# Optimization experiments

Measured on AMD Instinct MI355X. Metric: run time of the kernel, lower is better.

Reference implementation:

```python
import jax, jax.numpy as jnp
import numpy as np

F = 3          # features
E = 2 * F      # transformer d_model
H = F          # n_heads (head_dim = 2)
FF = 2048      # torch TransformerEncoderLayer default dim_feedforward
OUT = 4
STRIDE = 2
N_BATCH = 16
T_LEN = 2046
LN_EPS = 1e-5


def setup_inputs() -> dict:
    key = jax.random.key(0)
    ks = iter(jax.random.split(key, 48))

    def p(shape, s=0.1):
        return jax.random.normal(next(ks), shape, dtype=jnp.float32) * s

    inp = {
        "x": jax.random.normal(next(ks), (N_BATCH, T_LEN, F), dtype=jnp.float32),
        # multi-scale depthwise conv kernels/biases
        "k64": p((8, F, 64)), "b64": p((8, F)),
        "k16": p((F, 16)), "b16": p((F,)),
        "k8": p((F, 8)), "b8": p((F,)),
        # stage-2 width-3 channel convs
        "kw3": p((F, 3)), "bw3": p((F,)),
        "km3": p((F, 3)), "bm3": p((F,)),
        "kn3": p((F, 3)), "bn3": p((F,)),
        # hidden FCs
        "fc1_w": p((6 * F, 12 * F)), "fc1_b": p((6 * F,)),
        "fc2_w": p((E, 6 * F)), "fc2_b": p((E,)),
        # 2 transformer encoder layers (stacked along leading dim)
        "inw": p((2, 3 * E, E)), "inb": p((2, 3 * E)),
        "ow": p((2, E, E)), "ob": p((2, E)),
        "l1w": jnp.ones((2, E), jnp.float32), "l1b": jnp.zeros((2, E), jnp.float32),
        "l2w": jnp.ones((2, E), jnp.float32), "l2b": jnp.zeros((2, E), jnp.float32),
        "f1w": p((2, FF, E)), "f1b": p((2, FF)),
        "f2w": p((2, E, FF)), "f2b": p((2, E)),
        # output head
        "out1_w": p((7, E)), "out1_b": p((7,)),
        "out2_w": p((OUT, 7)),
    }
    return inp


def _ln(y, w, b):
    mu = y.mean(-1, keepdims=True)
    var = ((y - mu) ** 2).mean(-1, keepdims=True)
    return (y - mu) / jnp.sqrt(var + LN_EPS) * w + b


def _conv3_same(y, k, b):
    # depthwise width-3 'same' conv over seq dim; y:(N,L,F), k:(F,3), b:(F,)
    yp = jnp.pad(y, ((0, 0), (1, 1), (0, 0)))
    return k[:, 0] * yp[:, :-2] + k[:, 1] * yp[:, 1:-1] + k[:, 2] * yp[:, 2:] + b


def _forward(x, k64, b64, k16, b16, k8, b8, kw3, bw3, km3, bm3, kn3, bn3,
             fc1_w, fc1_b, fc2_w, fc2_b, inw, inb, ow, ob,
             l1w, l1b, l2w, l2b, f1w, f1b, f2w, f2b, out1_w, out1_b, out2_w):
    N, T, _ = x.shape
    PAD = 40
    px = jnp.pad(x, ((0, 0), (PAD, PAD), (0, 0)))
    W = T // STRIDE + 1
    centers = PAD + 1 + STRIDE * jnp.arange(W)  # wide window centers
    starts = centers - 32
    relu = jax.nn.relu

    # wide: 8 depthwise width-64 kernels per center -> (N, 8W, F)
    wwin = px[:, centers[:, None] + jnp.arange(-32, 32), :]        # (N,W,64,F)
    wide = jnp.einsum('nwtf,kft->nwkf', wwin, k64) + b64[None, None]
    wide = wide.reshape(N, 8 * W, F)  # center-major, kernel-minor (loop order)

    # mid: width-16 kernel at 8 centers per window -> (N, 8W, F)
    mid_c = (starts[:, None] + 8 * jnp.arange(8)).reshape(-1)
    mwin = px[:, mid_c[:, None] + jnp.arange(-8, 8), :]            # (N,8W,16,F)
    mid = jnp.einsum('nctf,ft->ncf', mwin, k16) + b16

    # narrow: width-8 kernel at 32 centers per window, then maxpool4 -> (N, 8W, F)
    nar_c = (starts[:, None] + 2 * jnp.arange(32)).reshape(-1)
    nwin = px[:, nar_c[:, None] + jnp.arange(-4, 4), :]            # (N,32W,8,F)
    nar = jnp.einsum('nctf,ft->ncf', nwin, k8) + b8
    nar = nar.reshape(N, 8 * W, 4, F).max(axis=2)

    wide = 5.0 * relu(wide)  # residual=0, dropout=0 -> drop is identity
    mid = relu(mid)
    nar = relu(nar)

    wide = relu(_conv3_same(wide, kw3, bw3))
    mid = relu(_conv3_same(mid, km3, bm3))
    nar = relu(_conv3_same(nar, kn3, bn3))

    def pool2(y):  # MaxPool1d(2) over seq dim
        return y.reshape(N, 4 * W, 2, F).max(axis=2)
    wide, mid, nar = pool2(wide), pool2(mid), pool2(nar)

    S = W  # (4W) // 4 blocks

    def blocks(y):  # (N,4W,F) -> (N,S,4F), time-major flatten per block
        return y.reshape(N, S, 4 * F)
    flat = jnp.concatenate([blocks(wide), blocks(mid), blocks(nar)], axis=-1)

    h = relu(flat @ fc1_w.T + fc1_b)  # residual=0 -> (1-residual)*h + 0
    h = relu(h @ fc2_w.T + fc2_b)     # (N,S,E)
    seq = jnp.transpose(h, (1, 0, 2))  # (S,N,E), torch seq-first layout

    d = E // H
    scale = 1.0 / jnp.sqrt(jnp.float32(d))
    for l in range(2):  # post-LN TransformerEncoder, 2 layers
        qkv = seq @ inw[l].T + inb[l]                 # (S,N,3E)
        q, k_, v = jnp.split(qkv, 3, axis=-1)
        q = q.reshape(S, N, H, d)
        k_ = k_.reshape(S, N, H, d)
        v = v.reshape(S, N, H, d)
        att = jnp.einsum('snhd,tnhd->nhst', q, k_) * scale
        p_att = jax.nn.softmax(att, axis=-1)
        o = jnp.einsum('nhst,tnhd->snhd', p_att, v).reshape(S, N, E)
        o = o @ ow[l].T + ob[l]
        seq = _ln(seq + o, l1w[l], l1b[l])
        ff = relu(seq @ f1w[l].T + f1b[l]) @ f2w[l].T + f2b[l]
        seq = _ln(seq + ff, l2w[l], l2b[l])

    pooled = relu(seq.mean(axis=0))           # AvgPool1d over full seq -> (N,E)
    o1 = relu(pooled @ out1_w.T + out1_b)
    logits = o1 @ out2_w.T                    # no bias
    return jax.nn.log_softmax(logits, axis=1)


def reference(x, k64, b64, k16, b16, k8, b8, kw3, bw3, km3, bm3, kn3, bn3,
              fc1_w, fc1_b, fc2_w, fc2_b, inw, inb, ow, ob,
              l1w, l1b, l2w, l2b, f1w, f1b, f2w, f2b, out1_w, out1_b, out2_w):
    return _forward(x, k64, b64, k16, b16, k8, b8, kw3, bw3, km3, bm3, kn3, bn3,
                    fc1_w, fc1_b, fc2_w, fc2_b, inw, inb, ow, ob,
                    l1w, l1b, l2w, l2b, f1w, f1b, f2w, f2b, out1_w, out1_b, out2_w)
```

## Files before the change

kernel.cpp:

```cpp
#include <hip/hip_runtime.h>
#include <math.h>


#define NB 16
#define TL 2046
#define SL 1024
#define ED 6

__device__ __forceinline__ float relu_(float a){ return fmaxf(a, 0.f); }
__device__ __forceinline__ float fexp2_(float x){ return __builtin_amdgcn_exp2f(x); }

__global__ __launch_bounds__(192) void frontend_kernel(
  const float* __restrict__ x, const float* __restrict__ k64,
  const float* __restrict__ b64, const float* __restrict__ k16, const float* __restrict__ b16,
  const float* __restrict__ k8,  const float* __restrict__ b8,
  const float* __restrict__ kw3, const float* __restrict__ bw3,
  const float* __restrict__ km3, const float* __restrict__ bm3,
  const float* __restrict__ kn3, const float* __restrict__ bn3,
  const float* __restrict__ fc1w, const float* __restrict__ fc1b,
  const float* __restrict__ fc2w, const float* __restrict__ fc2b,
  const float* __restrict__ f1w, const float* __restrict__ f1b,
  const float* __restrict__ f2w,
  float* __restrict__ fcc, float* __restrict__ seq)
{
  __shared__ float xt[3][200];
  __shared__ float k64s[3*64*8];
  __shared__ float flat_s[64][44];
  __shared__ float h1_s[64][20];
  const int tid  = threadIdx.x;
  const int f    = tid >> 6;
  const int lane = tid & 63;
  const int n    = blockIdx.x >> 4;
  const int s0   = (blockIdx.x & 15) << 6;
  const int s    = s0 + lane;

  for (int i = blockIdx.x*192 + tid; i < 2*2048*16; i += 256*192){
    int l = i >> 15, r = i & 32767, j = r >> 4, c = r & 15;
    float v = 0.f;
    if (c < 6)       v = f1w[(l*2048 + j)*6 + c];
    else if (c == 6) v = f1b[l*2048 + j];
    else if (c >= 8 && c < 14) v = f2w[(l*6 + (c-8))*2048 + j];
    fcc[i] = v;
  }

  for (int i = tid; i < 600; i += 192){
    int ff = i / 200, pos = i - ff*200;
    int xp = 2*s0 - 39 + pos;
    xt[ff][pos] = (xp >= 0 && xp < TL) ? x[(n*TL + xp)*3 + ff] : 0.f;
  }
  for (int i = tid; i < 1536; i += 192){
    int ff = i >> 9, r = i & 511, t = r >> 3, k = r & 7;
    k64s[i] = k64[k*192 + ff*64 + t];
  }
  __syncthreads();

  float xr[74];
  {
    const int b = 2*lane;
    #pragma unroll
    for (int i = 0; i < 74; i++) xr[i] = xt[f][b + i];
  }

  float accw[8], acc_e0, acc_e1;
  #pragma unroll
  for (int k = 0; k < 8; k++) accw[k] = b64[k*3 + f];
  acc_e0 = accw[7]; acc_e1 = accw[0];
  {
    const float* kp = &k64s[f*512];
    #pragma unroll
    for (int t = 0; t < 64; t++){
      float4 wa = *(const float4*)(kp + t*8);
      float4 wb = *(const float4*)(kp + t*8 + 4);
      float xm = xr[8 + t];
      accw[0] = fmaf(xm, wa.x, accw[0]);
      accw[1] = fmaf(xm, wa.y, accw[1]);
      accw[2] = fmaf(xm, wa.z, accw[2]);
      accw[3] = fmaf(xm, wa.w, accw[3]);
      accw[4] = fmaf(xm, wb.x, accw[4]);
      accw[5] = fmaf(xm, wb.y, accw[5]);
      accw[6] = fmaf(xm, wb.z, accw[6]);
      accw[7] = fmaf(xm, wb.w, accw[7]);
      acc_e0 = fmaf(xr[6 + t],  wb.w, acc_e0);
      acc_e1 = fmaf(xr[10 + t], wa.x, acc_e1);
    }
  }
  float yw[10];
  yw[0] = (s > 0) ? 5.f*relu_(acc_e0) : 0.f;
  #pragma unroll
  for (int c = 1; c <= 8; c++) yw[c] = 5.f*relu_(accw[c-1]);
  yw[9] = (s < 1023) ? 5.f*relu_(acc_e1) : 0.f;

  float w16r[16];
  #pragma unroll
  for (int t = 0; t < 16; t++) w16r[t] = k16[f*16 + t];
  const float bb16 = b16[f];
  float ym[10];
  #pragma unroll
  for (int ci = 0; ci < 10; ci++){
    const int b = (ci == 0) ? 54 : ((ci == 9) ? 2 : 8*(ci-1));
    float a = bb16;
    #pragma unroll
    for (int t = 0; t < 16; t++) a = fmaf(xr[b + t], w16r[t], a);
    ym[ci] = relu_(a);
  }
  if (s == 0)    ym[0] = 0.f;
  if (s == 1023) ym[9] = 0.f;

  float w8r[8];
  #pragma unroll
  for (int t = 0; t < 8; t++) w8r[t] = k8[f*8 + t];
  const float bb8 = b8[f];
  float yn[10];
  #pragma unroll
  for (int ci = 0; ci < 10; ci++){
    float m = -3.0e38f;
    #pragma unroll
    for (int j2 = 0; j2 < 4; j2++){
      const int b = (ci == 0) ? (58 + 2*j2)
                  : ((ci == 9) ? (6 + 2*j2)
                               : (4 + 2*(4*(ci-1) + j2)));
      float a = bb8;
      #pragma unroll
      for (int t = 0; t < 8; t++) a = fmaf(xr[b + t], w8r[t], a);
      m = fmaxf(m, a);
    }
    yn[ci] = relu_(m);
  }
  if (s == 0)    yn[0] = 0.f;
  if (s == 1023) yn[9] = 0.f;

  {
    float c0 = kw3[f*3], c1 = kw3[f*3+1], c2 = kw3[f*3+2], bb = bw3[f];
    #pragma unroll
    for (int q = 0; q < 4; q++){
      float z0 = relu_(fmaf(c0, yw[2*q],   fmaf(c1, yw[2*q+1], fmaf(c2, yw[2*q+2], bb))));
      float z1 = relu_(fmaf(c0, yw[2*q+1], fmaf(c1, yw[2*q+2], fmaf(c2, yw[2*q+3], bb))));
      flat_s[lane][q*3 + f] = fmaxf(z0, z1);
    }
  }
  {
    float c0 = km3[f*3], c1 = km3[f*3+1], c2 = km3[f*3+2], bb = bm3[f];
    #pragma unroll
    for (int q = 0; q < 4; q++){
      float z0 = relu_(fmaf(c0, ym[2*q],   fmaf(c1, ym[2*q+1], fmaf(c2, ym[2*q+2], bb))));
      float z1 = relu_(fmaf(c0, ym[2*q+1], fmaf(c1, ym[2*q+2], fmaf(c2, ym[2*q+3], bb))));
      flat_s[lane][12 + q*3 + f] = fmaxf(z0, z1);
    }
  }
  {
    float c0 = kn3[f*3], c1 = kn3[f*3+1], c2 = kn3[f*3+2], bb = bn3[f];
    #pragma unroll
    for (int q = 0; q < 4; q++){
      float z0 = relu_(fmaf(c0, yn[2*q],   fmaf(c1, yn[2*q+1], fmaf(c2, yn[2*q+2], bb))));
      float z1 = relu_(fmaf(c0, yn[2*q+1], fmaf(c1, yn[2*q+2], fmaf(c2, yn[2*q+3], bb))));
      flat_s[lane][24 + q*3 + f] = fmaxf(z0, z1);
    }
  }
  __syncthreads();

  #pragma unroll
  for (int oi = 0; oi < 6; oi++){
    const int o = 6*f + oi;
    float acc = fc1b[o];
    const float4* wrow = (const float4*)(fc1w + o*36);
    const float4* frow = (const float4*)(&flat_s[lane][0]);
    #pragma unroll
    for (int i = 0; i < 9; i++){
      float4 wv = wrow[i], fv = frow[i];
      acc = fmaf(wv.x, fv.x, acc); acc = fmaf(wv.y, fv.y, acc);
      acc = fmaf(wv.z, fv.z, acc); acc = fmaf(wv.w, fv.w, acc);
    }
    h1_s[lane][o] = relu_(acc);
  }
  __syncthreads();

  #pragma unroll
  for (int ei = 0; ei < 2; ei++){
    const int e = 2*f + ei;
    float acc = fc2b[e];
    #pragma unroll
    for (int o = 0; o < 18; o++) acc = fmaf(h1_s[lane][o], fc2w[e*18 + o], acc);
    seq[(n*SL + s)*ED + e] = relu_(acc);
  }
}

__global__ __launch_bounds__(256) void attn_kernel(
  const float* __restrict__ seq, const float* __restrict__ inw,
  const float* __restrict__ inb, float* __restrict__ att_out, int layer)
{
  __shared__ float4 kv[1024];
  const int tid = threadIdx.x;
  const int bid = blockIdx.x;
  const int n = bid / 48;
  const int r = bid % 48;
  const int h = r >> 4;
  const int stile = r & 15;
  const float* W = inw + layer*108;
  const float* B = inb + layer*18;
  const int h2 = 2*h;
  const float* seqn = seq + n*SL*ED;
  const float SC = 1.0201265650432017f;

  float wk0[6], wk1[6], wv0[6], wv1[6];
  #pragma unroll
  for (int e = 0; e < 6; e++){
    wk0[e] = W[(6 + h2)*6 + e];  wk1[e] = W[(7 + h2)*6 + e];
    wv0[e] = W[(12 + h2)*6 + e]; wv1[e] = W[(13 + h2)*6 + e];
  }
  const float bk0 = B[6 + h2], bk1 = B[7 + h2], bv0 = B[12 + h2], bv1 = B[13 + h2];

  for (int i = tid; i < 1024; i += 256){
    const int t = (i & 3)*256 + (i >> 2);
    const float* sr = seqn + t*6;
    float a0 = sr[0], a1 = sr[1], a2 = sr[2], a3 = sr[3], a4 = sr[4], a5 = sr[5];
    float k0 = bk0 + a0*wk0[0] + a1*wk0[1] + a2*wk0[2] + a3*wk0[3] + a4*wk0[4] + a5*wk0[5];
    float k1 = bk1 + a0*wk1[0] + a1*wk1[1] + a2*wk1[2] + a3*wk1[3] + a4*wk1[4] + a5*wk1[5];
    float v0 = bv0 + a0*wv0[0] + a1*wv0[1] + a2*wv0[2] + a3*wv0[3] + a4*wv0[4] + a5*wv0[5];
    float v1 = bv1 + a0*wv1[0] + a1*wv1[1] + a2*wv1[2] + a3*wv1[3] + a4*wv1[4] + a5*wv1[5];
    kv[i] = make_float4(k0*SC, k1*SC, v0, v1);
  }

  const int srow = stile*64 + (tid >> 2);
  const int q = tid & 3;
  float q0, q1;
  {
    const float* sr = seqn + srow*6;
    float a0 = sr[0], a1 = sr[1], a2 = sr[2], a3 = sr[3], a4 = sr[4], a5 = sr[5];
    q0 = B[h2]   + a0*W[h2*6]     + a1*W[h2*6+1]     + a2*W[h2*6+2]     + a3*W[h2*6+3]     + a4*W[h2*6+4]     + a5*W[h2*6+5];
    q1 = B[h2+1] + a0*W[(h2+1)*6] + a1*W[(h2+1)*6+1] + a2*W[(h2+1)*6+2] + a3*W[(h2+1)*6+3] + a4*W[(h2+1)*6+4] + a5*W[(h2+1)*6+5];
  }
  __syncthreads();

  float l = 0.f, o0 = 0.f, o1 = 0.f;
  #pragma unroll 8
  for (int it = 0; it < 256; it++){
    float4 K = kv[it*4 + q];
    float sc = fmaf(q0, K.x, q1*K.y);
    float p  = fexp2_(sc);
    l += p;
    o0 = fmaf(p, K.z, o0);
    o1 = fmaf(p, K.w, o1);
  }
  l  += __shfl_xor(l, 1);  l  += __shfl_xor(l, 2);
  o0 += __shfl_xor(o0, 1); o0 += __shfl_xor(o0, 2);
  o1 += __shfl_xor(o1, 1); o1 += __shfl_xor(o1, 2);
  if (q == 0){
    float inv = 1.0f / l;
    float* orow = att_out + (n*SL + srow)*ED + h2;
    orow[0] = o0*inv; orow[1] = o1*inv;
  }
}

__global__ __launch_bounds__(256) void ff_kernel(
  const float* __restrict__ seq_in, const float* __restrict__ att,
  const float* __restrict__ fcc,
  const float* __restrict__ ow, const float* __restrict__ ob,
  const float* __restrict__ l1w, const float* __restrict__ l1b,
  float* __restrict__ seq_mid, float* __restrict__ ffp, int layer)
{
  __shared__ float wc[512][16];
  __shared__ float sM[128][6];
  const int tid   = threadIdx.x;
  const int tile  = blockIdx.x >> 2;
  const int slice = blockIdx.x & 3;
  const int tok0  = tile * 128;

  const float4* FC = (const float4*)(fcc + (size_t)(layer*2048 + slice*512)*16);
  for (int i = tid; i < 2048; i += 256)
    ((float4*)wc)[i] = FC[i];

  if (tid < 128){
    const int token = tok0 + tid;
    const float* a  = att + token*6;
    const float* W  = ow + layer*36;
    float av[6];
    #pragma unroll
    for (int e = 0; e < 6; e++) av[e] = a[e];
    float y[6]; float mu = 0.f;
    #pragma unroll
    for (int e = 0; e < 6; e++){
      float o = ob[layer*6 + e];
      #pragma unroll
      for (int e2 = 0; e2 < 6; e2++) o = fmaf(av[e2], W[e*6 + e2], o);
      y[e] = seq_in[token*6 + e] + o;
      mu += y[e];
    }
    mu *= (1.f/6.f);
    float var = 0.f;
    #pragma unroll
    for (int e = 0; e < 6; e++){ float d = y[e] - mu; var = fmaf(d, d, var); }
    var *= (1.f/6.f);
    float rstd = rsqrtf(var + 1e-5f);
    #pragma unroll
    for (int e = 0; e < 6; e++)
      sM[tid][e] = (y[e] - mu)*rstd*l1w[layer*6 + e] + l1b[layer*6 + e];
  }
  __syncthreads();

  const int w = tid >> 6, lane = tid & 63, tp = lane >> 2, ss = lane & 3;

  float sv[8][6];
  {
    const float* sp = &sM[tp*8][0];
    #pragma unroll
    for (int t = 0; t < 8; t++)
      #pragma unroll
      for (int e = 0; e < 6; e++) sv[t][e] = sp[t*6 + e];
  }
  float acc[8][6];
  #pragma unroll
  for (int t = 0; t < 8; t++)
    #pragma unroll
    for (int e = 0; e < 6; e++) acc[t][e] = 0.f;

  const int rb = w*128 + ss;
  #pragma unroll 2
  for (int i = 0; i < 32; i++){
    const float4* wr = (const float4*)&wc[rb + i*4][0];
    float4 w0 = wr[0], w1 = wr[1], w2 = wr[2], w3 = wr[3];
    #pragma unroll
    for (int t = 0; t < 8; t++){
      float h = w1.z;
      h = fmaf(sv[t][0], w0.x, h); h = fmaf(sv[t][1], w0.y, h);
      h = fmaf(sv[t][2], w0.z, h); h = fmaf(sv[t][3], w0.w, h);
      h = fmaf(sv[t][4], w1.x, h); h = fmaf(sv[t][5], w1.y, h);
      h = relu_(h);
      acc[t][0] = fmaf(h, w2.x, acc[t][0]); acc[t][1] = fmaf(h, w2.y, acc[t][1]);
      acc[t][2] = fmaf(h, w2.z, acc[t][2]); acc[t][3] = fmaf(h, w2.w, acc[t][3]);
      acc[t][4] = fmaf(h, w3.x, acc[t][4]); acc[t][5] = fmaf(h, w3.y, acc[t][5]);
    }
  }

  #pragma unroll
  for (int t = 0; t < 8; t++)
    #pragma unroll
    for (int e = 0; e < 6; e++){
      acc[t][e] += __shfl_xor(acc[t][e], 1);
      acc[t][e] += __shfl_xor(acc[t][e], 2);
    }
  __syncthreads();
  float* red = (float*)wc;
  if (ss == 0){
    #pragma unroll
    for (int t = 0; t < 8; t++)
      #pragma unroll
      for (int e = 0; e < 6; e++) red[(w*16 + tp)*48 + t*6 + e] = acc[t][e];
  }
  __syncthreads();
  for (int i = tid; i < 768; i += 256){
    const int tl = i / 6, e = i - tl*6;
    const int rtp = tl >> 3, rt = tl & 7;
    float sum = red[(0*16 + rtp)*48 + rt*6 + e]
              + red[(1*16 + rtp)*48 + rt*6 + e]
              + red[(2*16 + rtp)*48 + rt*6 + e]
              + red[(3*16 + rtp)*48 + rt*6 + e];
    ffp[(size_t)(slice*16384 + tok0 + tl)*6 + e] = sum;
  }
  if (slice == 0 && tid < 128){
    #pragma unroll
    for (int e = 0; e < 6; e++) seq_mid[(tok0 + tid)*6 + e] = sM[tid][e];
  }
}

__global__ __launch_bounds__(128) void ffln_kernel(
  const float* __restrict__ seq_mid, const float* __restrict__ ffp,
  const float* __restrict__ f2b, const float* __restrict__ lw,
  const float* __restrict__ lb, float* __restrict__ seq_out, int layer)
{
  const int tok = blockIdx.x*128 + threadIdx.x;
  float y[6]; float mu = 0.f;
  #pragma unroll
  for (int e = 0; e < 6; e++){
    float v = seq_mid[tok*6 + e] + f2b[layer*6 + e];
    v += ffp[(size_t)(0*16384 + tok)*6 + e];
    v += ffp[(size_t)(1*16384 + tok)*6 + e];
    v += ffp[(size_t)(2*16384 + tok)*6 + e];
    v += ffp[(size_t)(3*16384 + tok)*6 + e];
    y[e] = v; mu += v;
  }
  mu *= (1.f/6.f);
  float var = 0.f;
  #pragma unroll
  for (int e = 0; e < 6; e++){ float d = y[e] - mu; var = fmaf(d, d, var); }
  var *= (1.f/6.f);
  float rstd = rsqrtf(var + 1e-5f);
  #pragma unroll
  for (int e = 0; e < 6; e++)
    seq_out[tok*6 + e] = (y[e] - mu)*rstd*lw[layer*6 + e] + lb[layer*6 + e];
}

__global__ __launch_bounds__(192) void final_kernel(
  const float* __restrict__ seq, const float* __restrict__ o1w,
  const float* __restrict__ o1b, const float* __restrict__ o2w,
  float* __restrict__ out)
{
  __shared__ float red[6][33];
  __shared__ float pooled[6];
  const int n = blockIdx.x, tid = threadIdx.x, e = tid >> 5, ch = tid & 31;
  float s = 0.f;
  for (int i = ch; i < 1024; i += 32) s += seq[(n*SL + i)*ED + e];
  red[e][ch] = s;
  __syncthreads();
  if (tid < 6){
    float t = 0.f;
    for (int i = 0; i < 32; i++) t += red[tid][i];
    pooled[tid] = fmaxf(t * (1.f/1024.f), 0.f);
  }
  __syncthreads();
  if (tid == 0){
    float o1[7];
    #pragma unroll
    for (int o = 0; o < 7; o++){
      float a = o1b[o];
      #pragma unroll
      for (int e2 = 0; e2 < 6; e2++) a = fmaf(pooled[e2], o1w[o*6 + e2], a);
      o1[o] = relu_(a);
    }
    float lg[4];
    #pragma unroll
    for (int c = 0; c < 4; c++){
      float a = 0.f;
      #pragma unroll
      for (int o = 0; o < 7; o++) a = fmaf(o1[o], o2w[c*7 + o], a);
      lg[c] = a;
    }
    float m = fmaxf(fmaxf(lg[0], lg[1]), fmaxf(lg[2], lg[3]));
    float sum = 0.f;
    #pragma unroll
    for (int c = 0; c < 4; c++) sum += expf(lg[c] - m);
    float lse = m + logf(sum);
    #pragma unroll
    for (int c = 0; c < 4; c++) out[n*4 + c] = lg[c] - lse;
  }
}

extern "C" void kernel_launch(void* const* d_in, const int* in_sizes, int n_in,
                              void* d_out, int out_size, void* d_ws, size_t ws_size,
                              hipStream_t stream)
{
  const float* x    = (const float*)d_in[0];
  const float* k64  = (const float*)d_in[1];
  const float* b64  = (const float*)d_in[2];
  const float* k16  = (const float*)d_in[3];
  const float* b16  = (const float*)d_in[4];
  const float* k8   = (const float*)d_in[5];
  const float* b8   = (const float*)d_in[6];
  const float* kw3  = (const float*)d_in[7];
  const float* bw3  = (const float*)d_in[8];
  const float* km3  = (const float*)d_in[9];
  const float* bm3  = (const float*)d_in[10];
  const float* kn3  = (const float*)d_in[11];
  const float* bn3  = (const float*)d_in[12];
  const float* fc1w = (const float*)d_in[13];
  const float* fc1b = (const float*)d_in[14];
  const float* fc2w = (const float*)d_in[15];
  const float* fc2b = (const float*)d_in[16];
  const float* inw  = (const float*)d_in[17];
  const float* inb  = (const float*)d_in[18];
  const float* ow   = (const float*)d_in[19];
  const float* ob   = (const float*)d_in[20];
  const float* l1w  = (const float*)d_in[21];
  const float* l1b  = (const float*)d_in[22];
  const float* l2w  = (const float*)d_in[23];
  const float* l2b  = (const float*)d_in[24];
  const float* f1w  = (const float*)d_in[25];
  const float* f1b  = (const float*)d_in[26];
  const float* f2w  = (const float*)d_in[27];
  const float* f2b  = (const float*)d_in[28];
  const float* o1w  = (const float*)d_in[29];
  const float* o1b  = (const float*)d_in[30];
  const float* o2w  = (const float*)d_in[31];
  float* out = (float*)d_out;

  float* w = (float*)d_ws;
  float* seq_a   = w;
  float* seq_b   = w + 98304;
  float* att     = w + 196608;
  float* seq_mid = w + 294912;
  float* ffp     = w + 393216;
  float* fcc     = w + 786432;

  frontend_kernel<<<256, 192, 0, stream>>>(x, k64, b64, k16, b16, k8, b8,
      kw3, bw3, km3, bm3, kn3, bn3, fc1w, fc1b, fc2w, fc2b,
      f1w, f1b, f2w, fcc, seq_a);
  attn_kernel<<<768, 256, 0, stream>>>(seq_a, inw, inb, att, 0);
  ff_kernel<<<512, 256, 0, stream>>>(seq_a, att, fcc, ow, ob, l1w, l1b,
      seq_mid, ffp, 0);
  ffln_kernel<<<128, 128, 0, stream>>>(seq_mid, ffp, f2b, l2w, l2b, seq_b, 0);
  attn_kernel<<<768, 256, 0, stream>>>(seq_b, inw, inb, att, 1);
  ff_kernel<<<512, 256, 0, stream>>>(seq_b, att, fcc, ow, ob, l1w, l1b,
      seq_mid, ffp, 1);
  ffln_kernel<<<128, 128, 0, stream>>>(seq_mid, ffp, f2b, l2w, l2b, seq_a, 1);
  final_kernel<<<16, 192, 0, stream>>>(seq_a, o1w, o1b, o2w, out);
}
```

Measured before the change: 88.82 us.

## Precompute QKV in producer kernels, register-block attention rows, fuse final LayerNorm into pooling

Frontend and the layer-0 post-FF LayerNorm kernel now compute per-head Q and scaled K/V directly and write them to dedicated buffers. The attention kernel no longer recomputes projections per block; instead each thread keeps 16 query rows in registers and reuses each shared-memory K/V load across them, with a shuffle-plus-LDS reduction. The last LayerNorm is folded into the pooling kernel, dropping one launch and a round trip of the sequence. This costs higher register pressure in attention and extra global writes in producers.

```diff
diff --git a/kernel.cpp b/kernel.cpp
--- a/kernel.cpp
+++ b/kernel.cpp
@@ -9,6 +9,8 @@
 
 __device__ __forceinline__ float relu_(float a){ return fmaxf(a, 0.f); }
 __device__ __forceinline__ float fexp2_(float x){ return __builtin_amdgcn_exp2f(x); }
+
+#define SCQK 1.0201265650432017f
 
 __global__ __launch_bounds__(192) void frontend_kernel(
   const float* __restrict__ x, const float* __restrict__ k64,
@@ -21,12 +23,15 @@
   const float* __restrict__ fc2w, const float* __restrict__ fc2b,
   const float* __restrict__ f1w, const float* __restrict__ f1b,
   const float* __restrict__ f2w,
-  float* __restrict__ fcc, float* __restrict__ seq)
+  const float* __restrict__ inw, const float* __restrict__ inb,
+  float* __restrict__ fcc, float* __restrict__ seq,
+  float4* __restrict__ kv4, float2* __restrict__ qq)
 {
   __shared__ float xt[3][200];
   __shared__ float k64s[3*64*8];
   __shared__ float flat_s[64][44];
   __shared__ float h1_s[64][20];
+  __shared__ float seq6[64][6];
   const int tid  = threadIdx.x;
   const int f    = tid >> 6;
   const int lane = tid & 63;
@@ -180,74 +185,113 @@
     float acc = fc2b[e];
     #pragma unroll
     for (int o = 0; o < 18; o++) acc = fmaf(h1_s[lane][o], fc2w[e*18 + o], acc);
-    seq[(n*SL + s)*ED + e] = relu_(acc);
+    seq[(n*SL + s)*ED + e] = acc < 0.f ? 0.f : acc;
+    seq6[lane][e] = acc < 0.f ? 0.f : acc;
+  }
+  __syncthreads();
+
+  {
+    const int g = f;
+    float sv[6];
+    #pragma unroll
+    for (int e = 0; e < 6; e++) sv[e] = seq6[lane][e];
+    const float* W = inw;
+    const float* B = inb;
+    const int h2 = 2*g;
+    float q0 = B[h2],   q1 = B[h2+1];
+    float k0 = B[6+h2], k1 = B[7+h2];
+    float v0 = B[12+h2], v1 = B[13+h2];
+    #pragma unroll
+    for (int e = 0; e < 6; e++){
+      q0 = fmaf(sv[e], W[h2*6 + e],      q0);
+      q1 = fmaf(sv[e], W[(h2+1)*6 + e],  q1);
+      k0 = fmaf(sv[e], W[(6+h2)*6 + e],  k0);
+      k1 = fmaf(sv[e], W[(7+h2)*6 + e],  k1);
+      v0 = fmaf(sv[e], W[(12+h2)*6 + e], v0);
+      v1 = fmaf(sv[e], W[(13+h2)*6 + e], v1);
+    }
+    const int nh = n*3 + g;
+    kv4[nh*SL + s] = make_float4(k0*SCQK, k1*SCQK, v0, v1);
+    qq [nh*SL + s] = make_float2(q0, q1);
   }
 }
 
 __global__ __launch_bounds__(256) void attn_kernel(
-  const float* __restrict__ seq, const float* __restrict__ inw,
-  const float* __restrict__ inb, float* __restrict__ att_out, int layer)
+  const float4* __restrict__ kv4, const float2* __restrict__ qq,
+  float* __restrict__ att_out)
 {
-  __shared__ float4 kv[1024];
-  const int tid = threadIdx.x;
-  const int bid = blockIdx.x;
-  const int n = bid / 48;
-  const int r = bid % 48;
-  const int h = r >> 4;
-  const int stile = r & 15;
-  const float* W = inw + layer*108;
-  const float* B = inb + layer*18;
-  const int h2 = 2*h;
-  const float* seqn = seq + n*SL*ED;
-  const float SC = 1.0201265650432017f;
-
-  float wk0[6], wk1[6], wv0[6], wv1[6];
-  #pragma unroll
-  for (int e = 0; e < 6; e++){
-    wk0[e] = W[(6 + h2)*6 + e];  wk1[e] = W[(7 + h2)*6 + e];
-    wv0[e] = W[(12 + h2)*6 + e]; wv1[e] = W[(13 + h2)*6 + e];
-  }
-  const float bk0 = B[6 + h2], bk1 = B[7 + h2], bv0 = B[12 + h2], bv1 = B[13 + h2];
-
-  for (int i = tid; i < 1024; i += 256){
-    const int t = (i & 3)*256 + (i >> 2);
-    const float* sr = seqn + t*6;
-    float a0 = sr[0], a1 = sr[1], a2 = sr[2], a3 = sr[3], a4 = sr[4], a5 = sr[5];
-    float k0 = bk0 + a0*wk0[0] + a1*wk0[1] + a2*wk0[2] + a3*wk0[3] + a4*wk0[4] + a5*wk0[5];
-    float k1 = bk1 + a0*wk1[0] + a1*wk1[1] + a2*wk1[2] + a3*wk1[3] + a4*wk1[4] + a5*wk1[5];
-    float v0 = bv0 + a0*wv0[0] + a1*wv0[1] + a2*wv0[2] + a3*wv0[3] + a4*wv0[4] + a5*wv0[5];
-    float v1 = bv1 + a0*wv1[0] + a1*wv1[1] + a2*wv1[2] + a3*wv1[3] + a4*wv1[4] + a5*wv1[5];
-    kv[i] = make_float4(k0*SC, k1*SC, v0, v1);
-  }
-
-  const int srow = stile*64 + (tid >> 2);
-  const int q = tid & 3;
-  float q0, q1;
-  {
-    const float* sr = seqn + srow*6;
-    float a0 = sr[0], a1 = sr[1], a2 = sr[2], a3 = sr[3], a4 = sr[4], a5 = sr[5];
-    q0 = B[h2]   + a0*W[h2*6]     + a1*W[h2*6+1]     + a2*W[h2*6+2]     + a3*W[h2*6+3]     + a4*W[h2*6+4]     + a5*W[h2*6+5];
-    q1 = B[h2+1] + a0*W[(h2+1)*6] + a1*W[(h2+1)*6+1] + a2*W[(h2+1)*6+2] + a3*W[(h2+1)*6+3] + a4*W[(h2+1)*6+4] + a5*W[(h2+1)*6+5];
-  }
-  __syncthreads();
-
-  float l = 0.f, o0 = 0.f, o1 = 0.f;
-  #pragma unroll 8
-  for (int it = 0; it < 256; it++){
-    float4 K = kv[it*4 + q];
-    float sc = fmaf(q0, K.x, q1*K.y);
-    float p  = fexp2_(sc);
-    l += p;
-    o0 = fmaf(p, K.z, o0);
-    o1 = fmaf(p, K.w, o1);
-  }
-  l  += __shfl_xor(l, 1);  l  += __shfl_xor(l, 2);
-  o0 += __shfl_xor(o0, 1); o0 += __shfl_xor(o0, 2);
-  o1 += __shfl_xor(o1, 1); o1 += __shfl_xor(o1, 2);
-  if (q == 0){
-    float inv = 1.0f / l;
-    float* orow = att_out + (n*SL + srow)*ED + h2;
-    orow[0] = o0*inv; orow[1] = o1*inv;
+  __shared__ float4 sKV[1024];
+  __shared__ float red[4][8][16][3];
+  const int tid  = threadIdx.x;
+  const int w    = tid >> 6;
+  const int lane = tid & 63;
+  const int rb   = blockIdx.x << 6;
+  const int h    = blockIdx.y;
+  const int n    = blockIdx.z;
+  const int nh   = n*3 + h;
+
+  const float4* kvp = kv4 + nh*SL;
+  #pragma unroll
+  for (int i = 0; i < 4; i++) sKV[tid + i*256] = kvp[tid + i*256];
+
+  const int r0 = rb + w*16;
+  float q0[16], q1[16];
+  {
+    const float2* qp = qq + nh*SL + r0;
+    #pragma unroll
+    for (int r = 0; r < 16; r++){ float2 qv = qp[r]; q0[r] = qv.x; q1[r] = qv.y; }
+  }
+  __syncthreads();
+
+  float l[16], o0[16], o1[16];
+  #pragma unroll
+  for (int r = 0; r < 16; r++){ l[r] = 0.f; o0[r] = 0.f; o1[r] = 0.f; }
+
+  #pragma unroll 2
+  for (int i = 0; i < 16; i++){
+    float4 K = sKV[i*64 + lane];
+    #pragma unroll
+    for (int r = 0; r < 16; r++){
+      float sc = fmaf(q0[r], K.x, q1[r]*K.y);
+      float p  = fexp2_(sc);
+      l[r] += p;
+      o0[r] = fmaf(p, K.z, o0[r]);
+      o1[r] = fmaf(p, K.w, o1[r]);
+    }
+  }
+
+  #pragma unroll
+  for (int r = 0; r < 16; r++){
+    l[r]  += __shfl_xor(l[r], 1);  l[r]  += __shfl_xor(l[r], 2);  l[r]  += __shfl_xor(l[r], 4);
+    o0[r] += __shfl_xor(o0[r], 1); o0[r] += __shfl_xor(o0[r], 2); o0[r] += __shfl_xor(o0[r], 4);
+    o1[r] += __shfl_xor(o1[r], 1); o1[r] += __shfl_xor(o1[r], 2); o1[r] += __shfl_xor(o1[r], 4);
+  }
+  {
+    const int g = lane >> 3;
+    #pragma unroll
+    for (int r = 0; r < 16; r++){
+      if ((lane & 7) == (r & 7)){
+        red[w][g][r][0] = l[r];
+        red[w][g][r][1] = o0[r];
+        red[w][g][r][2] = o1[r];
+      }
+    }
+  }
+  __syncthreads();
+
+  if (tid < 64){
+    const int ww = tid >> 4, r = tid & 15;
+    float L = 0.f, O0 = 0.f, O1 = 0.f;
+    #pragma unroll
+    for (int g = 0; g < 8; g++){
+      L  += red[ww][g][r][0];
+      O0 += red[ww][g][r][1];
+      O1 += red[ww][g][r][2];
+    }
+    const int row = rb + ww*16 + r;
+    const float inv = 1.0f / L;
+    float* orow = att_out + (n*SL + row)*ED + 2*h;
+    orow[0] = O0*inv; orow[1] = O1*inv;
   }
 }
 
@@ -365,13 +409,15 @@
 __global__ __launch_bounds__(128) void ffln_kernel(
   const float* __restrict__ seq_mid, const float* __restrict__ ffp,
   const float* __restrict__ f2b, const float* __restrict__ lw,
-  const float* __restrict__ lb, float* __restrict__ seq_out, int layer)
+  const float* __restrict__ lb,
+  const float* __restrict__ Wq, const float* __restrict__ Bq,
+  float* __restrict__ seq_out, float4* __restrict__ kv4, float2* __restrict__ qq)
 {
   const int tok = blockIdx.x*128 + threadIdx.x;
   float y[6]; float mu = 0.f;
   #pragma unroll
   for (int e = 0; e < 6; e++){
-    float v = seq_mid[tok*6 + e] + f2b[layer*6 + e];
+    float v = seq_mid[tok*6 + e] + f2b[e];
     v += ffp[(size_t)(0*16384 + tok)*6 + e];
     v += ffp[(size_t)(1*16384 + tok)*6 + e];
     v += ffp[(size_t)(2*16384 + tok)*6 + e];
@@ -384,26 +430,84 @@
   for (int e = 0; e < 6; e++){ float d = y[e] - mu; var = fmaf(d, d, var); }
   var *= (1.f/6.f);
   float rstd = rsqrtf(var + 1e-5f);
-  #pragma unroll
-  for (int e = 0; e < 6; e++)
-    seq_out[tok*6 + e] = (y[e] - mu)*rstd*lw[layer*6 + e] + lb[layer*6 + e];
+  float sv[6];
+  #pragma unroll
+  for (int e = 0; e < 6; e++){
+    sv[e] = (y[e] - mu)*rstd*lw[e] + lb[e];
+    seq_out[tok*6 + e] = sv[e];
+  }
+
+  const int n = tok >> 10, t = tok & 1023;
+  #pragma unroll
+  for (int g = 0; g < 3; g++){
+    const int h2 = 2*g;
+    float q0 = Bq[h2],   q1 = Bq[h2+1];
+    float k0 = Bq[6+h2], k1 = Bq[7+h2];
+    float v0 = Bq[12+h2], v1 = Bq[13+h2];
+    #pragma unroll
+    for (int e = 0; e < 6; e++){
+      q0 = fmaf(sv[e], Wq[h2*6 + e],      q0);
+      q1 = fmaf(sv[e], Wq[(h2+1)*6 + e],  q1);
+      k0 = fmaf(sv[e], Wq[(6+h2)*6 + e],  k0);
+      k1 = fmaf(sv[e], Wq[(7+h2)*6 + e],  k1);
+      v0 = fmaf(sv[e], Wq[(12+h2)*6 + e], v0);
+      v1 = fmaf(sv[e], Wq[(13+h2)*6 + e], v1);
+    }
+    const int nh = n*3 + g;
+    kv4[nh*SL + t] = make_float4(k0*SCQK, k1*SCQK, v0, v1);
+    qq [nh*SL + t] = make_float2(q0, q1);
+  }
 }
 
-__global__ __launch_bounds__(192) void final_kernel(
-  const float* __restrict__ seq, const float* __restrict__ o1w,
-  const float* __restrict__ o1b, const float* __restrict__ o2w,
-  float* __restrict__ out)
+__global__ __launch_bounds__(256) void final_kernel(
+  const float* __restrict__ seq_mid, const float* __restrict__ ffp,
+  const float* __restrict__ f2b, const float* __restrict__ lw,
+  const float* __restrict__ lb,
+  const float* __restrict__ o1w, const float* __restrict__ o1b,
+  const float* __restrict__ o2w, float* __restrict__ out)
 {
-  __shared__ float red[6][33];
+  __shared__ float fred[4][6];
   __shared__ float pooled[6];
-  const int n = blockIdx.x, tid = threadIdx.x, e = tid >> 5, ch = tid & 31;
-  float s = 0.f;
-  for (int i = ch; i < 1024; i += 32) s += seq[(n*SL + i)*ED + e];
-  red[e][ch] = s;
+  const int n = blockIdx.x, tid = threadIdx.x;
+  float psum[6] = {0,0,0,0,0,0};
+
+  #pragma unroll
+  for (int i = 0; i < 4; i++){
+    const int tok = n*SL + tid + i*256;
+    float y[6]; float mu = 0.f;
+    #pragma unroll
+    for (int e = 0; e < 6; e++){
+      float v = seq_mid[tok*6 + e] + f2b[e];
+      v += ffp[(size_t)(0*16384 + tok)*6 + e];
+      v += ffp[(size_t)(1*16384 + tok)*6 + e];
+      v += ffp[(size_t)(2*16384 + tok)*6 + e];
+      v += ffp[(size_t)(3*16384 + tok)*6 + e];
+      y[e] = v; mu += v;
+    }
+    mu *= (1.f/6.f);
+    float var = 0.f;
+    #pragma unroll
+    for (int e = 0; e < 6; e++){ float d = y[e] - mu; var = fmaf(d, d, var); }
+    var *= (1.f/6.f);
+    float rstd = rsqrtf(var + 1e-5f);
+    #pragma unroll
+    for (int e = 0; e < 6; e++)
+      psum[e] += (y[e] - mu)*rstd*lw[e] + lb[e];
+  }
+
+  #pragma unroll
+  for (int e = 0; e < 6; e++){
+    psum[e] += __shfl_xor(psum[e], 1);  psum[e] += __shfl_xor(psum[e], 2);
+    psum[e] += __shfl_xor(psum[e], 4);  psum[e] += __shfl_xor(psum[e], 8);
+    psum[e] += __shfl_xor(psum[e], 16); psum[e] += __shfl_xor(psum[e], 32);
+  }
+  if ((tid & 63) == 0){
+    #pragma unroll
+    for (int e = 0; e < 6; e++) fred[tid >> 6][e] = psum[e];
+  }
   __syncthreads();
   if (tid < 6){
-    float t = 0.f;
-    for (int i = 0; i < 32; i++) t += red[tid][i];
+    float t = fred[0][tid] + fred[1][tid] + fred[2][tid] + fred[3][tid];
     pooled[tid] = fmaxf(t * (1.f/1024.f), 0.f);
   }
   __syncthreads();
@@ -473,23 +577,29 @@
   float* out = (float*)d_out;
 
   float* w = (float*)d_ws;
-  float* seq_a   = w;
-  float* seq_b   = w + 98304;
-  float* att     = w + 196608;
-  float* seq_mid = w + 294912;
-  float* ffp     = w + 393216;
-  float* fcc     = w + 786432;
+  float*  seq_a   = w;
+  float*  seq_b   = w + 98304;
+  float*  att     = w + 196608;
+  float*  seq_mid = w + 294912;
+  float*  ffp     = w + 393216;
+  float*  fcc     = w + 786432;
+  float4* kv4     = (float4*)(w + 851968);
+  float2* qq      = (float2*)(w + 1048576);
 
   frontend_kernel<<<256, 192, 0, stream>>>(x, k64, b64, k16, b16, k8, b8,
       kw3, bw3, km3, bm3, kn3, bn3, fc1w, fc1b, fc2w, fc2b,
-      f1w, f1b, f2w, fcc, seq_a);
-  attn_kernel<<<768, 256, 0, stream>>>(seq_a, inw, inb, att, 0);
+      f1w, f1b, f2w, inw, inb, fcc, seq_a, kv4, qq);
+
+  dim3 agrid(16, 3, 16);
+  attn_kernel<<<agrid, 256, 0, stream>>>(kv4, qq, att);
   ff_kernel<<<512, 256, 0, stream>>>(seq_a, att, fcc, ow, ob, l1w, l1b,
       seq_mid, ffp, 0);
-  ffln_kernel<<<128, 128, 0, stream>>>(seq_mid, ffp, f2b, l2w, l2b, seq_b, 0);
-  attn_kernel<<<768, 256, 0, stream>>>(seq_b, inw, inb, att, 1);
+  ffln_kernel<<<128, 128, 0, stream>>>(seq_mid, ffp, f2b, l2w, l2b,
+      inw + 108, inb + 18, seq_b, kv4, qq);
+
+  attn_kernel<<<agrid, 256, 0, stream>>>(kv4, qq, att);
   ff_kernel<<<512, 256, 0, stream>>>(seq_b, att, fcc, ow, ob, l1w, l1b,
       seq_mid, ffp, 1);
-  ffln_kernel<<<128, 128, 0, stream>>>(seq_mid, ffp, f2b, l2w, l2b, seq_a, 1);
-  final_kernel<<<16, 192, 0, stream>>>(seq_a, o1w, o1b, o2w, out);
+  final_kernel<<<16, 256, 0, stream>>>(seq_mid, ffp, f2b + 6, l2w + 6, l2b + 6,
+      o1w, o1b, o2w, out);
 }
```

New measurement: 82.36 us. 1.08x faster.
